# Performance work log

Hardware: AMD Instinct MI355X
Metric: run time of the kernel (lower is better)

Reference implementation:

```python
import jax, jax.numpy as jnp
import numpy as np

B, S, D, E, H, TOPK = 4, 2048, 1024, 32, 128, 4

def setup_inputs() -> dict:
    key = jax.random.key(0)
    k1, k2, k3, k4 = jax.random.split(key, 4)
    x = jax.random.normal(k1, (B, S, D), jnp.float32)
    expert_sel = jax.random.normal(k2, (E, D), jnp.float32) * (D ** -0.5)
    keys = jax.random.normal(k3, (E, D, H), jnp.float32) * (D ** -0.5)
    values = jax.random.normal(k4, (E, H, D), jnp.float32) * (H ** -0.5)
    return {"x": x, "expert_sel": expert_sel, "keys": keys, "values": values, "n_heads": TOPK}

def reference(x, expert_sel, keys, values, n_heads):
    # x: [B,S,D]; expert_sel: [E,D]; keys: [E,D,H]; values: [E,H,D]
    Bv, Sv, Dv = x.shape
    Ev = keys.shape[0]
    xf = x.reshape(-1, Dv)                                  # [N,D]
    N = xf.shape[0]
    gate = jax.nn.sigmoid(xf @ expert_sel.T)                # [N,E] sigmoid gating (sigma-MoE)
    vals, idx = jax.lax.top_k(gate, n_heads)                # [N,k] selected experts + gate weights
    # dense per-token-per-expert gate weights; zero for non-selected experts
    g = jnp.zeros((N, Ev), x.dtype).at[jnp.arange(N)[:, None], idx].set(vals)  # [N,E]
    # grouped expert FFN, expressed densely over the (small) expert axis:
    # out = sum_e g[n,e] * relu(x @ keys[e]) @ values[e]
    h = jax.nn.relu(jnp.einsum('nd,edh->enh', xf, keys))    # [E,N,H]
    out = jnp.einsum('enh,ehd->nd', h * g.T[:, :, None], values)  # [N,D]
    return out.reshape(Bv, Sv, Dv)
```

## Files before the change

kernel.cpp:

```cpp
#include <hip/hip_runtime.h>
#include <hip/hip_bf16.h>

#define NTOK 8192
#define DDIM 1024
#define NEXP 32
#define HDIM 128
#define TOPK 4

typedef __attribute__((ext_vector_type(8))) short bf16x8;
typedef __attribute__((ext_vector_type(4))) float f32x4;

typedef unsigned int uint_g __attribute__((address_space(1)));
typedef unsigned int uint_l __attribute__((address_space(3)));

__device__ __forceinline__ void async_cp16(const void* g, void* l) {
    __builtin_amdgcn_global_load_lds((const uint_g*)g, (uint_l*)l, 16, 0, 0);
}

__device__ inline unsigned short f2bf(float f) {
    unsigned int u = __builtin_bit_cast(unsigned int, f);
    unsigned int r = (u + 0x7fffu + ((u >> 16) & 1u)) >> 16;
    return (unsigned short)r;
}
__device__ inline float bf2f(unsigned short s) {
    unsigned int u = ((unsigned int)s) << 16;
    return __builtin_bit_cast(float, u);
}

__global__ __launch_bounds__(256) void prep_weights(
    const float* __restrict__ x,
    const float* __restrict__ keys, const float* __restrict__ values,
    unsigned short* __restrict__ Kb, unsigned short* __restrict__ Vb,
    unsigned short* __restrict__ Xb)
{
    int idx = blockIdx.x * 256 + threadIdx.x;
    unsigned short o[8];
    if (idx < NEXP * 128 * 128) {
        int n = idx & 127, k0 = (idx >> 7) & 127, e = idx >> 14;
        const float* s = keys + ((size_t)e * DDIM + k0 * 8) * HDIM + n;
        #pragma unroll
        for (int j = 0; j < 8; ++j) o[j] = f2bf(s[(size_t)j * HDIM]);
        *(uint4*)&Kb[(size_t)idx * 8] = *(uint4*)o;
    } else if (idx < 2 * NEXP * 128 * 128) {
        idx -= NEXP * 128 * 128;
        int n = idx & 1023, k0 = (idx >> 10) & 15, e = idx >> 14;
        const float* s = values + ((size_t)e * HDIM + k0 * 8) * DDIM + n;
        #pragma unroll
        for (int j = 0; j < 8; ++j) o[j] = f2bf(s[(size_t)j * DDIM]);
        *(uint4*)&Vb[(size_t)idx * 8] = *(uint4*)o;
    } else {
        idx -= 2 * NEXP * 128 * 128;
        const float* s = x + (size_t)idx * 8;
        #pragma unroll
        for (int j = 0; j < 8; ++j) o[j] = f2bf(s[j]);
        *(uint4*)&Xb[(size_t)idx * 8] = *(uint4*)o;
    }
}

__global__ __launch_bounds__(256) void gate_partial(
    const float* __restrict__ x, const float* __restrict__ es,
    float* __restrict__ gpart)
{
    const int n0    = blockIdx.x * 16;
    const int dbase = blockIdx.y * 256;
    const int tid   = threadIdx.x;

    __shared__ float smem[4608];
    float* Xt  = smem;
    float* Est = smem + 64 * 36;

    const int t4  = (tid & 3) * 4;
    const int e4  = ((tid >> 2) & 7) * 4;
    const int rep = tid >> 5;

    const int xr = tid & 15, xc4 = (tid >> 4) * 4;
    const int er = tid & 31, ec8 = (tid >> 5) * 8;

    float acc[4][4] = {};

    for (int dc = dbase; dc < dbase + 256; dc += 64) {
        __syncthreads();
        {
            float4 v = *(const float4*)&x[(size_t)(n0 + xr) * DDIM + dc + xc4];
            Xt[(xc4 + 0) * 36 + xr] = v.x; Xt[(xc4 + 1) * 36 + xr] = v.y;
            Xt[(xc4 + 2) * 36 + xr] = v.z; Xt[(xc4 + 3) * 36 + xr] = v.w;
        }
        #pragma unroll
        for (int i = 0; i < 2; ++i) {
            float4 v = *(const float4*)&es[(size_t)er * DDIM + dc + ec8 + i * 4];
            Est[(ec8 + i * 4 + 0) * 36 + er] = v.x;
            Est[(ec8 + i * 4 + 1) * 36 + er] = v.y;
            Est[(ec8 + i * 4 + 2) * 36 + er] = v.z;
            Est[(ec8 + i * 4 + 3) * 36 + er] = v.w;
        }
        __syncthreads();

        #pragma unroll
        for (int s = 0; s < 8; ++s) {
            int d = s * 8 + rep;
            float4 xv = *(const float4*)&Xt[d * 36 + t4];
            float4 ev = *(const float4*)&Est[d * 36 + e4];
            const float xa[4] = {xv.x, xv.y, xv.z, xv.w};
            const float ea[4] = {ev.x, ev.y, ev.z, ev.w};
            #pragma unroll
            for (int i = 0; i < 4; ++i)
                #pragma unroll
                for (int j = 0; j < 4; ++j)
                    acc[i][j] = fmaf(xa[i], ea[j], acc[i][j]);
        }
    }

    __syncthreads();
    float* Lp = smem;
    #pragma unroll
    for (int i = 0; i < 4; ++i)
        #pragma unroll
        for (int j = 0; j < 4; ++j)
            Lp[(rep * 16 + t4 + i) * 33 + e4 + j] = acc[i][j];
    __syncthreads();

    for (int p = tid; p < 16 * 32; p += 256) {
        int tok = p >> 5, e = p & 31;
        float s = 0.f;
        #pragma unroll
        for (int r = 0; r < 8; ++r) s += Lp[(r * 16 + tok) * 33 + e];
        gpart[((size_t)blockIdx.y * NTOK + n0 + tok) * NEXP + e] = s;
    }
}

__global__ __launch_bounds__(256) void topk_scatter(
    const float* __restrict__ gpart,
    int* __restrict__ cnt, int* __restrict__ tok_list, float* __restrict__ gates)
{
    const int tid = threadIdx.x;
    const int n   = blockIdx.x * 256 + tid;

    __shared__ int hist[NEXP];
    __shared__ int bbase[NEXP];
    if (tid < NEXP) hist[tid] = 0;

    float lg[NEXP];
    #pragma unroll
    for (int i = 0; i < 8; ++i) {
        float4 v = *(const float4*)&gpart[(size_t)n * NEXP + i * 4];
        lg[i*4+0] = v.x; lg[i*4+1] = v.y; lg[i*4+2] = v.z; lg[i*4+3] = v.w;
    }
    #pragma unroll
    for (int j = 1; j < 4; ++j)
        #pragma unroll
        for (int i = 0; i < 8; ++i) {
            float4 v = *(const float4*)&gpart[((size_t)j * NTOK + n) * NEXP + i * 4];
            lg[i*4+0] += v.x; lg[i*4+1] += v.y; lg[i*4+2] += v.z; lg[i*4+3] += v.w;
        }

    int sel[TOPK]; float sv[TOPK];
    #pragma unroll
    for (int j = 0; j < TOPK; ++j) {
        float bv = -3.0e38f; int bi = 0;
        #pragma unroll
        for (int e = 0; e < NEXP; ++e) {
            bool taken = false;
            #pragma unroll
            for (int q = 0; q < j; ++q) taken = taken || (sel[q] == e);
            float v = taken ? -3.0e38f : lg[e];
            if (v > bv) { bv = v; bi = e; }
        }
        sel[j] = bi; sv[j] = bv;
    }

    __syncthreads();
    int lpos[TOPK];
    #pragma unroll
    for (int j = 0; j < TOPK; ++j) {
        gates[n * TOPK + j] = 1.f / (1.f + expf(-sv[j]));
        lpos[j] = atomicAdd(&hist[sel[j]], 1);
    }
    __syncthreads();
    if (tid < NEXP) bbase[tid] = atomicAdd(&cnt[tid], hist[tid]);
    __syncthreads();
    #pragma unroll
    for (int j = 0; j < TOPK; ++j)
        tok_list[(size_t)sel[j] * NTOK + bbase[sel[j]] + lpos[j]] = n * TOPK + j;
}

__global__ __launch_bounds__(256) void ffn_fused(
    const unsigned short* __restrict__ Xb,
    const unsigned short* __restrict__ Kb,
    const unsigned short* __restrict__ Vb,
    const int* __restrict__ cnt, const int* __restrict__ tok_list,
    const float* __restrict__ gates,
    unsigned short* __restrict__ Ob)
{
    const int bid = blockIdx.x;
    const int e = bid & 31, tile = bid >> 5;
    const int c = cnt[e], base = tile * 64;
    if (base >= c) return;
    const int nt   = min(64, c - base);
    const int tid  = threadIdx.x, wave = tid >> 6, lane = tid & 63;
    const int lm   = lane & 15, quad = lane >> 4;
    const int r2   = (wave >> 1) * 32;
    const int c2   = (wave & 1) * 64;
    const int cw   = (wave & 1) * 32;

    __shared__ __align__(16) unsigned short KV[8192];
    __shared__ __align__(16) unsigned short XO[4608];
    __shared__ __align__(16) unsigned short Hs[64 * 140];
    __shared__ int slot[64]; __shared__ int gtok[64]; __shared__ float gs[64];

    if (tid < 64) {
        if (tid < nt) {
            int v = tok_list[(size_t)e * NTOK + base + tid];
            slot[tid] = v; gtok[tid] = v >> 2; gs[tid] = gates[v];
        } else { slot[tid] = -1; gtok[tid] = 0; gs[tid] = 0.f; }
    }
    __syncthreads();

    const unsigned short* Ke    = Kb + (size_t)e * 131072;
    const unsigned short* Ve    = Vb + (size_t)e * 131072;
    const unsigned short* xrowb = Xb + (size_t)gtok[lane] * DDIM;

    f32x4 acc[2][4];
    #pragma unroll
    for (int i = 0; i < 2; ++i)
        #pragma unroll
        for (int j = 0; j < 4; ++j) acc[i][j] = (f32x4){0.f, 0.f, 0.f, 0.f};

    auto stageA = [&](int t) {
        int dc = t * 64;
        #pragma unroll
        for (int i = 0; i < 4; ++i) {
            int p = wave * 4 + i;
            async_cp16(Ke + ((size_t)(dc / 8 + (p >> 1)) * 128 + (p & 1) * 64 + lane) * 8,
                       &KV[p * 512]);
        }
        #pragma unroll
        for (int i = 0; i < 2; ++i) {
            int k0 = wave * 2 + i;
            async_cp16(xrowb + dc + k0 * 8, &XO[k0 * 512]);
        }
    };

    stageA(0);
    __syncthreads();

    for (int t = 0; t < 16; ++t) {
        #pragma unroll
        for (int ks = 0; ks < 2; ++ks) {
            int k0 = ks * 4 + quad;
            bf16x8 a0 = *(const bf16x8*)&XO[(k0 * 64 + r2 + lm) * 8];
            bf16x8 a1 = *(const bf16x8*)&XO[(k0 * 64 + r2 + 16 + lm) * 8];
            #pragma unroll
            for (int tj = 0; tj < 4; ++tj) {
                bf16x8 bb = *(const bf16x8*)&KV[(k0 * 128 + c2 + tj * 16 + lm) * 8];
                acc[0][tj] = __builtin_amdgcn_mfma_f32_16x16x32_bf16(a0, bb, acc[0][tj], 0, 0, 0);
                acc[1][tj] = __builtin_amdgcn_mfma_f32_16x16x32_bf16(a1, bb, acc[1][tj], 0, 0, 0);
            }
        }
        if (t < 15) {
            __syncthreads();
            stageA(t + 1);
            __syncthreads();
        }
    }

    #pragma unroll
    for (int ti = 0; ti < 2; ++ti)
        #pragma unroll
        for (int reg = 0; reg < 4; ++reg) {
            int m = r2 + ti * 16 + quad * 4 + reg;
            float g = gs[m];
            #pragma unroll
            for (int tj = 0; tj < 4; ++tj)
                Hs[m * 140 + c2 + tj * 16 + lm] = f2bf(fmaxf(acc[ti][tj][reg], 0.f) * g);
        }
    __syncthreads();

    auto stageV = [&](int cc) {
        #pragma unroll
        for (int i = 0; i < 4; ++i) {
            int p = wave * 4 + i;
            async_cp16(Ve + ((size_t)p * 1024 + cc * 64 + lane) * 8, &KV[p * 512]);
        }
    };

    stageV(0);
    __syncthreads();

    const int om = tid >> 2, oq = tid & 3;
    const int os = slot[om];

    for (int cc = 0; cc < 16; ++cc) {
        f32x4 acc2[2][2];
        #pragma unroll
        for (int i = 0; i < 2; ++i) {
            acc2[i][0] = (f32x4){0.f, 0.f, 0.f, 0.f};
            acc2[i][1] = (f32x4){0.f, 0.f, 0.f, 0.f};
        }

        #pragma unroll
        for (int ks = 0; ks < 4; ++ks) {
            int k0 = ks * 4 + quad;
            bf16x8 a0 = *(const bf16x8*)&Hs[(r2 + lm) * 140 + k0 * 8];
            bf16x8 a1 = *(const bf16x8*)&Hs[(r2 + 16 + lm) * 140 + k0 * 8];
            #pragma unroll
            for (int tj = 0; tj < 2; ++tj) {
                bf16x8 bb = *(const bf16x8*)&KV[(k0 * 64 + cw + tj * 16 + lm) * 8];
                acc2[0][tj] = __builtin_amdgcn_mfma_f32_16x16x32_bf16(a0, bb, acc2[0][tj], 0, 0, 0);
                acc2[1][tj] = __builtin_amdgcn_mfma_f32_16x16x32_bf16(a1, bb, acc2[1][tj], 0, 0, 0);
            }
        }

        #pragma unroll
        for (int ti = 0; ti < 2; ++ti)
            #pragma unroll
            for (int reg = 0; reg < 4; ++reg) {
                int m = r2 + ti * 16 + quad * 4 + reg;
                XO[m * 72 + cw + lm]      = f2bf(acc2[ti][0][reg]);
                XO[m * 72 + cw + 16 + lm] = f2bf(acc2[ti][1][reg]);
            }
        __syncthreads();

        if (os >= 0) {
            uint4 v0 = *(const uint4*)&XO[om * 72 + oq * 16];
            uint4 v1 = *(const uint4*)&XO[om * 72 + oq * 16 + 8];
            unsigned short* op = Ob + (size_t)os * DDIM + cc * 64 + oq * 16;
            *(uint4*)op       = v0;
            *(uint4*)(op + 8) = v1;
        }
        if (cc < 15) stageV(cc + 1);
        __syncthreads();
    }
}

__global__ __launch_bounds__(256) void reduce_out(
    const unsigned short* __restrict__ Ob, float* __restrict__ out)
{
    const int tid = threadIdx.x;
    const int n   = blockIdx.x * 2 + (tid >> 7);
    const int cc  = (tid & 127) * 8;

    float s[8] = {};
    #pragma unroll
    for (int j = 0; j < 4; ++j) {
        uint4 v = *(const uint4*)&Ob[((size_t)n * 4 + j) * DDIM + cc];
        const unsigned int w[4] = {v.x, v.y, v.z, v.w};
        #pragma unroll
        for (int q = 0; q < 4; ++q) {
            s[q * 2 + 0] += bf2f((unsigned short)(w[q] & 0xffff));
            s[q * 2 + 1] += bf2f((unsigned short)(w[q] >> 16));
        }
    }
    float4 o0 = {s[0], s[1], s[2], s[3]};
    float4 o1 = {s[4], s[5], s[6], s[7]};
    *(float4*)&out[(size_t)n * DDIM + cc]     = o0;
    *(float4*)&out[(size_t)n * DDIM + cc + 4] = o1;
}

extern "C" void kernel_launch(void* const* d_in, const int* in_sizes, int n_in,
                              void* d_out, int out_size, void* d_ws, size_t ws_size,
                              hipStream_t stream) {
    const float* x      = (const float*)d_in[0];
    const float* es     = (const float*)d_in[1];
    const float* keys   = (const float*)d_in[2];
    const float* values = (const float*)d_in[3];
    float* out          = (float*)d_out;

    char* w = (char*)d_ws;
    int*   cnt      = (int*)w;               w += 256;
    int*   tok_list = (int*)w;               w += (size_t)NEXP * NTOK * sizeof(int);
    float* gates    = (float*)w;             w += (size_t)NTOK * TOPK * sizeof(float);
    float* gpart    = (float*)w;             w += (size_t)4 * NTOK * NEXP * sizeof(float);
    unsigned short* Kb = (unsigned short*)w; w += (size_t)NEXP * 128 * 128 * 8 * 2;
    unsigned short* Vb = (unsigned short*)w; w += (size_t)NEXP * 16 * 1024 * 8 * 2;
    unsigned short* Xb = (unsigned short*)w; w += (size_t)NTOK * DDIM * 2;
    unsigned short* Ob = (unsigned short*)w;

    hipMemsetAsync(cnt, 0, NEXP * sizeof(int), stream);

    prep_weights<<<8192, 256, 0, stream>>>(x, keys, values, Kb, Vb, Xb);
    gate_partial<<<dim3(NTOK / 16, 4), 256, 0, stream>>>(x, es, gpart);
    topk_scatter<<<NTOK / 256, 256, 0, stream>>>(gpart, cnt, tok_list, gates);

    ffn_fused<<<128 * NEXP, 256, 0, stream>>>(Xb, Kb, Vb, cnt, tok_list, gates, Ob);
    reduce_out<<<NTOK / 2, 256, 0, stream>>>(Ob, out);
}
```

Baseline: 205.9 us.

## Double-buffer FFN stages, persistent expert tiles, fuse x bf16 cast into gating

The x-to-bf16 conversion moves out of prep_weights and into gate_partial, which already stages x in shared memory, so x is read from global memory once instead of twice. ffn_fused becomes persistent: 512 blocks each loop over tiles of one expert with a stride of 16, replacing the 4096-block grid where most blocks exited early. The K/X, V and output staging buffers are double-buffered in one shared arena, so async loads of the next chunk overlap the MFMA work and one barrier per step is removed. The larger shared footprint (about 76 KB) may lower occupancy, and the new buffer aliasing needs careful barrier placement.

```diff
diff --git a/kernel.cpp b/kernel.cpp
--- a/kernel.cpp
+++ b/kernel.cpp
@@ -28,10 +28,8 @@
 }
 
 __global__ __launch_bounds__(256) void prep_weights(
-    const float* __restrict__ x,
     const float* __restrict__ keys, const float* __restrict__ values,
-    unsigned short* __restrict__ Kb, unsigned short* __restrict__ Vb,
-    unsigned short* __restrict__ Xb)
+    unsigned short* __restrict__ Kb, unsigned short* __restrict__ Vb)
 {
     int idx = blockIdx.x * 256 + threadIdx.x;
     unsigned short o[8];
@@ -41,25 +39,20 @@
         #pragma unroll
         for (int j = 0; j < 8; ++j) o[j] = f2bf(s[(size_t)j * HDIM]);
         *(uint4*)&Kb[(size_t)idx * 8] = *(uint4*)o;
-    } else if (idx < 2 * NEXP * 128 * 128) {
+    } else {
         idx -= NEXP * 128 * 128;
         int n = idx & 1023, k0 = (idx >> 10) & 15, e = idx >> 14;
         const float* s = values + ((size_t)e * HDIM + k0 * 8) * DDIM + n;
         #pragma unroll
         for (int j = 0; j < 8; ++j) o[j] = f2bf(s[(size_t)j * DDIM]);
         *(uint4*)&Vb[(size_t)idx * 8] = *(uint4*)o;
-    } else {
-        idx -= 2 * NEXP * 128 * 128;
-        const float* s = x + (size_t)idx * 8;
-        #pragma unroll
-        for (int j = 0; j < 8; ++j) o[j] = f2bf(s[j]);
-        *(uint4*)&Xb[(size_t)idx * 8] = *(uint4*)o;
     }
 }
 
 __global__ __launch_bounds__(256) void gate_partial(
     const float* __restrict__ x, const float* __restrict__ es,
-    float* __restrict__ gpart)
+    float* __restrict__ gpart,
+    unsigned short* __restrict__ Xb)
 {
     const int n0    = blockIdx.x * 16;
     const int dbase = blockIdx.y * 256;
@@ -75,6 +68,8 @@
 
     const int xr = tid & 15, xc4 = (tid >> 4) * 4;
     const int er = tid & 31, ec8 = (tid >> 5) * 8;
+
+    const int ctok = tid >> 4, cd4 = (tid & 15) * 4;
 
     float acc[4][4] = {};
 
@@ -94,6 +89,13 @@
             Est[(ec8 + i * 4 + 3) * 36 + er] = v.w;
         }
         __syncthreads();
+
+        {
+            unsigned short o[4];
+            #pragma unroll
+            for (int j = 0; j < 4; ++j) o[j] = f2bf(Xt[(cd4 + j) * 36 + ctok]);
+            *(uint2*)&Xb[(size_t)(n0 + ctok) * DDIM + dc + cd4] = *(uint2*)o;
+        }
 
         #pragma unroll
         for (int s = 0; s < 8; ++s) {
@@ -192,122 +194,76 @@
     unsigned short* __restrict__ Ob)
 {
     const int bid = blockIdx.x;
-    const int e = bid & 31, tile = bid >> 5;
-    const int c = cnt[e], base = tile * 64;
-    if (base >= c) return;
-    const int nt   = min(64, c - base);
+    const int e = bid & 31, t0 = bid >> 5;
+    const int c = cnt[e];
     const int tid  = threadIdx.x, wave = tid >> 6, lane = tid & 63;
     const int lm   = lane & 15, quad = lane >> 4;
     const int r2   = (wave >> 1) * 32;
     const int c2   = (wave & 1) * 64;
     const int cw   = (wave & 1) * 32;
 
-    __shared__ __align__(16) unsigned short KV[8192];
-    __shared__ __align__(16) unsigned short XO[4608];
-    __shared__ __align__(16) unsigned short Hs[64 * 140];
+    __shared__ __align__(16) unsigned short P[37888];
     __shared__ int slot[64]; __shared__ int gtok[64]; __shared__ float gs[64];
 
-    if (tid < 64) {
-        if (tid < nt) {
-            int v = tok_list[(size_t)e * NTOK + base + tid];
-            slot[tid] = v; gtok[tid] = v >> 2; gs[tid] = gates[v];
-        } else { slot[tid] = -1; gtok[tid] = 0; gs[tid] = 0.f; }
-    }
-    __syncthreads();
-
-    const unsigned short* Ke    = Kb + (size_t)e * 131072;
-    const unsigned short* Ve    = Vb + (size_t)e * 131072;
-    const unsigned short* xrowb = Xb + (size_t)gtok[lane] * DDIM;
-
-    f32x4 acc[2][4];
-    #pragma unroll
-    for (int i = 0; i < 2; ++i)
-        #pragma unroll
-        for (int j = 0; j < 4; ++j) acc[i][j] = (f32x4){0.f, 0.f, 0.f, 0.f};
-
-    auto stageA = [&](int t) {
-        int dc = t * 64;
-        #pragma unroll
-        for (int i = 0; i < 4; ++i) {
-            int p = wave * 4 + i;
-            async_cp16(Ke + ((size_t)(dc / 8 + (p >> 1)) * 128 + (p & 1) * 64 + lane) * 8,
-                       &KV[p * 512]);
-        }
-        #pragma unroll
-        for (int i = 0; i < 2; ++i) {
-            int k0 = wave * 2 + i;
-            async_cp16(xrowb + dc + k0 * 8, &XO[k0 * 512]);
-        }
-    };
-
-    stageA(0);
-    __syncthreads();
-
-    for (int t = 0; t < 16; ++t) {
-        #pragma unroll
-        for (int ks = 0; ks < 2; ++ks) {
-            int k0 = ks * 4 + quad;
-            bf16x8 a0 = *(const bf16x8*)&XO[(k0 * 64 + r2 + lm) * 8];
-            bf16x8 a1 = *(const bf16x8*)&XO[(k0 * 64 + r2 + 16 + lm) * 8];
-            #pragma unroll
-            for (int tj = 0; tj < 4; ++tj) {
-                bf16x8 bb = *(const bf16x8*)&KV[(k0 * 128 + c2 + tj * 16 + lm) * 8];
-                acc[0][tj] = __builtin_amdgcn_mfma_f32_16x16x32_bf16(a0, bb, acc[0][tj], 0, 0, 0);
-                acc[1][tj] = __builtin_amdgcn_mfma_f32_16x16x32_bf16(a1, bb, acc[1][tj], 0, 0, 0);
-            }
-        }
-        if (t < 15) {
+    const unsigned short* Ke = Kb + (size_t)e * 131072;
+    const unsigned short* Ve = Vb + (size_t)e * 131072;
+
+    for (int tile = t0; tile * 64 < c; tile += 16) {
+        const int base = tile * 64;
+        const int nt   = min(64, c - base);
+
+        __syncthreads();
+        if (tid < 64) {
+            if (tid < nt) {
+                int v = tok_list[(size_t)e * NTOK + base + tid];
+                slot[tid] = v; gtok[tid] = v >> 2; gs[tid] = gates[v];
+            } else { slot[tid] = -1; gtok[tid] = 0; gs[tid] = 0.f; }
+        }
+        __syncthreads();
+
+        const unsigned short* xrowb = Xb + (size_t)gtok[lane] * DDIM;
+
+        f32x4 acc[2][4];
+        #pragma unroll
+        for (int i = 0; i < 2; ++i)
+            #pragma unroll
+            for (int j = 0; j < 4; ++j) acc[i][j] = (f32x4){0.f, 0.f, 0.f, 0.f};
+
+        auto stageA = [&](int t, int cb) {
+            unsigned short* B = &P[cb * 12288];
+            #pragma unroll
+            for (int i = 0; i < 4; ++i) {
+                int p = wave * 4 + i;
+                async_cp16(Ke + ((size_t)(t * 8 + (p >> 1)) * 128 + (p & 1) * 64 + lane) * 8,
+                           B + p * 512);
+            }
+            #pragma unroll
+            for (int i = 0; i < 2; ++i) {
+                int k0 = wave * 2 + i;
+                async_cp16(xrowb + t * 64 + k0 * 8, B + 8192 + k0 * 512);
+            }
+        };
+
+        stageA(0, 0);
+        __syncthreads();
+
+        for (int t = 0; t < 16; ++t) {
+            const int cb = t & 1;
+            if (t < 15) stageA(t + 1, cb ^ 1);
+            const unsigned short* B = &P[cb * 12288];
+            #pragma unroll
+            for (int ks = 0; ks < 2; ++ks) {
+                int k0 = ks * 4 + quad;
+                bf16x8 a0 = *(const bf16x8*)&B[8192 + (k0 * 64 + r2 + lm) * 8];
+                bf16x8 a1 = *(const bf16x8*)&B[8192 + (k0 * 64 + r2 + 16 + lm) * 8];
+                #pragma unroll
+                for (int tj = 0; tj < 4; ++tj) {
+                    bf16x8 bb = *(const bf16x8*)&B[(k0 * 128 + c2 + tj * 16 + lm) * 8];
+                    acc[0][tj] = __builtin_amdgcn_mfma_f32_16x16x32_bf16(a0, bb, acc[0][tj], 0, 0, 0);
+                    acc[1][tj] = __builtin_amdgcn_mfma_f32_16x16x32_bf16(a1, bb, acc[1][tj], 0, 0, 0);
+                }
+            }
             __syncthreads();
-            stageA(t + 1);
-            __syncthreads();
-        }
-    }
-
-    #pragma unroll
-    for (int ti = 0; ti < 2; ++ti)
-        #pragma unroll
-        for (int reg = 0; reg < 4; ++reg) {
-            int m = r2 + ti * 16 + quad * 4 + reg;
-            float g = gs[m];
-            #pragma unroll
-            for (int tj = 0; tj < 4; ++tj)
-                Hs[m * 140 + c2 + tj * 16 + lm] = f2bf(fmaxf(acc[ti][tj][reg], 0.f) * g);
-        }
-    __syncthreads();
-
-    auto stageV = [&](int cc) {
-        #pragma unroll
-        for (int i = 0; i < 4; ++i) {
-            int p = wave * 4 + i;
-            async_cp16(Ve + ((size_t)p * 1024 + cc * 64 + lane) * 8, &KV[p * 512]);
-        }
-    };
-
-    stageV(0);
-    __syncthreads();
-
-    const int om = tid >> 2, oq = tid & 3;
-    const int os = slot[om];
-
-    for (int cc = 0; cc < 16; ++cc) {
-        f32x4 acc2[2][2];
-        #pragma unroll
-        for (int i = 0; i < 2; ++i) {
-            acc2[i][0] = (f32x4){0.f, 0.f, 0.f, 0.f};
-            acc2[i][1] = (f32x4){0.f, 0.f, 0.f, 0.f};
-        }
-
-        #pragma unroll
-        for (int ks = 0; ks < 4; ++ks) {
-            int k0 = ks * 4 + quad;
-            bf16x8 a0 = *(const bf16x8*)&Hs[(r2 + lm) * 140 + k0 * 8];
-            bf16x8 a1 = *(const bf16x8*)&Hs[(r2 + 16 + lm) * 140 + k0 * 8];
-            #pragma unroll
-            for (int tj = 0; tj < 2; ++tj) {
-                bf16x8 bb = *(const bf16x8*)&KV[(k0 * 64 + cw + tj * 16 + lm) * 8];
-                acc2[0][tj] = __builtin_amdgcn_mfma_f32_16x16x32_bf16(a0, bb, acc2[0][tj], 0, 0, 0);
-                acc2[1][tj] = __builtin_amdgcn_mfma_f32_16x16x32_bf16(a1, bb, acc2[1][tj], 0, 0, 0);
-            }
         }
 
         #pragma unroll
@@ -315,20 +271,71 @@
             #pragma unroll
             for (int reg = 0; reg < 4; ++reg) {
                 int m = r2 + ti * 16 + quad * 4 + reg;
-                XO[m * 72 + cw + lm]      = f2bf(acc2[ti][0][reg]);
-                XO[m * 72 + cw + 16 + lm] = f2bf(acc2[ti][1][reg]);
-            }
-        __syncthreads();
-
-        if (os >= 0) {
-            uint4 v0 = *(const uint4*)&XO[om * 72 + oq * 16];
-            uint4 v1 = *(const uint4*)&XO[om * 72 + oq * 16 + 8];
-            unsigned short* op = Ob + (size_t)os * DDIM + cc * 64 + oq * 16;
-            *(uint4*)op       = v0;
-            *(uint4*)(op + 8) = v1;
-        }
-        if (cc < 15) stageV(cc + 1);
-        __syncthreads();
+                float g = gs[m];
+                #pragma unroll
+                for (int tj = 0; tj < 4; ++tj)
+                    P[m * 140 + c2 + tj * 16 + lm] = f2bf(fmaxf(acc[ti][tj][reg], 0.f) * g);
+            }
+
+        auto stageV = [&](int cc, int vb) {
+            unsigned short* B = &P[12288 + vb * 8192];
+            #pragma unroll
+            for (int i = 0; i < 4; ++i) {
+                int p = wave * 4 + i;
+                async_cp16(Ve + ((size_t)p * 1024 + cc * 64 + lane) * 8, B + p * 512);
+            }
+        };
+
+        stageV(0, 0);
+        __syncthreads();
+
+        const int om = tid >> 2, oq = tid & 3;
+        const int os = slot[om];
+
+        for (int cc = 0; cc < 16; ++cc) {
+            const int vb = cc & 1;
+            if (cc < 15) stageV(cc + 1, vb ^ 1);
+
+            f32x4 acc2[2][2];
+            #pragma unroll
+            for (int i = 0; i < 2; ++i) {
+                acc2[i][0] = (f32x4){0.f, 0.f, 0.f, 0.f};
+                acc2[i][1] = (f32x4){0.f, 0.f, 0.f, 0.f};
+            }
+
+            const unsigned short* B = &P[12288 + vb * 8192];
+            #pragma unroll
+            for (int ks = 0; ks < 4; ++ks) {
+                int k0 = ks * 4 + quad;
+                bf16x8 a0 = *(const bf16x8*)&P[(r2 + lm) * 140 + k0 * 8];
+                bf16x8 a1 = *(const bf16x8*)&P[(r2 + 16 + lm) * 140 + k0 * 8];
+                #pragma unroll
+                for (int tj = 0; tj < 2; ++tj) {
+                    bf16x8 bb = *(const bf16x8*)&B[(k0 * 64 + cw + tj * 16 + lm) * 8];
+                    acc2[0][tj] = __builtin_amdgcn_mfma_f32_16x16x32_bf16(a0, bb, acc2[0][tj], 0, 0, 0);
+                    acc2[1][tj] = __builtin_amdgcn_mfma_f32_16x16x32_bf16(a1, bb, acc2[1][tj], 0, 0, 0);
+                }
+            }
+
+            unsigned short* OSB = &P[28672 + vb * 4608];
+            #pragma unroll
+            for (int ti = 0; ti < 2; ++ti)
+                #pragma unroll
+                for (int reg = 0; reg < 4; ++reg) {
+                    int m = r2 + ti * 16 + quad * 4 + reg;
+                    OSB[m * 72 + cw + lm]      = f2bf(acc2[ti][0][reg]);
+                    OSB[m * 72 + cw + 16 + lm] = f2bf(acc2[ti][1][reg]);
+                }
+            __syncthreads();
+
+            if (os >= 0) {
+                uint4 v0 = *(const uint4*)&OSB[om * 72 + oq * 16];
+                uint4 v1 = *(const uint4*)&OSB[om * 72 + oq * 16 + 8];
+                unsigned short* op = Ob + (size_t)os * DDIM + cc * 64 + oq * 16;
+                *(uint4*)op       = v0;
+                *(uint4*)(op + 8) = v1;
+            }
+        }
     }
 }
 
@@ -377,10 +384,10 @@
 
     hipMemsetAsync(cnt, 0, NEXP * sizeof(int), stream);
 
-    prep_weights<<<8192, 256, 0, stream>>>(x, keys, values, Kb, Vb, Xb);
-    gate_partial<<<dim3(NTOK / 16, 4), 256, 0, stream>>>(x, es, gpart);
+    prep_weights<<<4096, 256, 0, stream>>>(keys, values, Kb, Vb);
+    gate_partial<<<dim3(NTOK / 16, 4), 256, 0, stream>>>(x, es, gpart, Xb);
     topk_scatter<<<NTOK / 256, 256, 0, stream>>>(gpart, cnt, tok_list, gates);
 
-    ffn_fused<<<128 * NEXP, 256, 0, stream>>>(Xb, Kb, Vb, cnt, tok_list, gates, Ob);
+    ffn_fused<<<512, 256, 0, stream>>>(Xb, Kb, Vb, cnt, tok_list, gates, Ob);
     reduce_out<<<NTOK / 2, 256, 0, stream>>>(Ob, out);
 }
```

After: 248.8 us. +20.8%, slower.

## Fuse weight prep, gate logits, top-k and scatter into one kernel

Applied to the files above, without the earlier changes.

Merges the weight conversion, gating GEMM and top-k/scatter kernels into a single launch. Weight-conversion blocks run alongside gate blocks, and each gate block now covers the full D dimension for 16 tokens. Each gate block also writes the bf16 copy of x while x is in shared memory. This removes the gpart partial-logit buffer round trip, two kernel launches and a separate pass over x. In exchange there are fewer gate blocks doing 4x more serial work each, and only 16 threads per block do the top-k, so the global atomics on cnt go from one batch per 256 tokens to one per 16 tokens.

```diff
diff --git a/kernel.cpp b/kernel.cpp
--- a/kernel.cpp
+++ b/kernel.cpp
@@ -27,47 +27,44 @@
     return __builtin_bit_cast(float, u);
 }
 
-__global__ __launch_bounds__(256) void prep_weights(
-    const float* __restrict__ x,
+__global__ __launch_bounds__(256) void prep_gate(
+    const float* __restrict__ x, const float* __restrict__ es,
     const float* __restrict__ keys, const float* __restrict__ values,
     unsigned short* __restrict__ Kb, unsigned short* __restrict__ Vb,
-    unsigned short* __restrict__ Xb)
+    unsigned short* __restrict__ Xb,
+    int* __restrict__ cnt, int* __restrict__ tok_list, float* __restrict__ gates)
 {
-    int idx = blockIdx.x * 256 + threadIdx.x;
-    unsigned short o[8];
-    if (idx < NEXP * 128 * 128) {
-        int n = idx & 127, k0 = (idx >> 7) & 127, e = idx >> 14;
-        const float* s = keys + ((size_t)e * DDIM + k0 * 8) * HDIM + n;
-        #pragma unroll
-        for (int j = 0; j < 8; ++j) o[j] = f2bf(s[(size_t)j * HDIM]);
-        *(uint4*)&Kb[(size_t)idx * 8] = *(uint4*)o;
-    } else if (idx < 2 * NEXP * 128 * 128) {
-        idx -= NEXP * 128 * 128;
-        int n = idx & 1023, k0 = (idx >> 10) & 15, e = idx >> 14;
-        const float* s = values + ((size_t)e * HDIM + k0 * 8) * DDIM + n;
-        #pragma unroll
-        for (int j = 0; j < 8; ++j) o[j] = f2bf(s[(size_t)j * DDIM]);
-        *(uint4*)&Vb[(size_t)idx * 8] = *(uint4*)o;
-    } else {
-        idx -= 2 * NEXP * 128 * 128;
-        const float* s = x + (size_t)idx * 8;
-        #pragma unroll
-        for (int j = 0; j < 8; ++j) o[j] = f2bf(s[j]);
-        *(uint4*)&Xb[(size_t)idx * 8] = *(uint4*)o;
-    }
-}
-
-__global__ __launch_bounds__(256) void gate_partial(
-    const float* __restrict__ x, const float* __restrict__ es,
-    float* __restrict__ gpart)
-{
-    const int n0    = blockIdx.x * 16;
-    const int dbase = blockIdx.y * 256;
-    const int tid   = threadIdx.x;
+    const int tid = threadIdx.x;
+
+    if (blockIdx.x < 4096) {
+        int idx = blockIdx.x * 256 + tid;
+        unsigned short o[8];
+        if (idx < NEXP * 128 * 128) {
+            int n = idx & 127, k0 = (idx >> 7) & 127, e = idx >> 14;
+            const float* s = keys + ((size_t)e * DDIM + k0 * 8) * HDIM + n;
+            #pragma unroll
+            for (int j = 0; j < 8; ++j) o[j] = f2bf(s[(size_t)j * HDIM]);
+            *(uint4*)&Kb[(size_t)idx * 8] = *(uint4*)o;
+        } else {
+            idx -= NEXP * 128 * 128;
+            int n = idx & 1023, k0 = (idx >> 10) & 15, e = idx >> 14;
+            const float* s = values + ((size_t)e * HDIM + k0 * 8) * DDIM + n;
+            #pragma unroll
+            for (int j = 0; j < 8; ++j) o[j] = f2bf(s[(size_t)j * DDIM]);
+            *(uint4*)&Vb[(size_t)idx * 8] = *(uint4*)o;
+        }
+        return;
+    }
+
+    const int n0 = (int)(blockIdx.x - 4096) * 16;
 
     __shared__ float smem[4608];
+    __shared__ float Ls[16 * 33];
+    __shared__ int hist[NEXP];
+    __shared__ int bbase[NEXP];
     float* Xt  = smem;
     float* Est = smem + 64 * 36;
+    float* Lp  = smem;
 
     const int t4  = (tid & 3) * 4;
     const int e4  = ((tid >> 2) & 7) * 4;
@@ -76,111 +73,111 @@
     const int xr = tid & 15, xc4 = (tid >> 4) * 4;
     const int er = tid & 31, ec8 = (tid >> 5) * 8;
 
-    float acc[4][4] = {};
-
-    for (int dc = dbase; dc < dbase + 256; dc += 64) {
+    const int ctok = tid >> 4, cd4 = (tid & 15) * 4;
+
+    const int rtok = tid >> 5, re = tid & 31;
+
+    float lsum[2] = {0.f, 0.f};
+
+    if (tid < NEXP) hist[tid] = 0;
+
+    for (int q = 0; q < 4; ++q) {
+        float acc[4][4] = {};
+
+        for (int dc = q * 256; dc < q * 256 + 256; dc += 64) {
+            __syncthreads();
+            {
+                float4 v = *(const float4*)&x[(size_t)(n0 + xr) * DDIM + dc + xc4];
+                Xt[(xc4 + 0) * 36 + xr] = v.x; Xt[(xc4 + 1) * 36 + xr] = v.y;
+                Xt[(xc4 + 2) * 36 + xr] = v.z; Xt[(xc4 + 3) * 36 + xr] = v.w;
+            }
+            #pragma unroll
+            for (int i = 0; i < 2; ++i) {
+                float4 v = *(const float4*)&es[(size_t)er * DDIM + dc + ec8 + i * 4];
+                Est[(ec8 + i * 4 + 0) * 36 + er] = v.x;
+                Est[(ec8 + i * 4 + 1) * 36 + er] = v.y;
+                Est[(ec8 + i * 4 + 2) * 36 + er] = v.z;
+                Est[(ec8 + i * 4 + 3) * 36 + er] = v.w;
+            }
+            __syncthreads();
+
+            {
+                unsigned short o[4];
+                #pragma unroll
+                for (int j = 0; j < 4; ++j) o[j] = f2bf(Xt[(cd4 + j) * 36 + ctok]);
+                *(uint2*)&Xb[(size_t)(n0 + ctok) * DDIM + dc + cd4] = *(uint2*)o;
+            }
+
+            #pragma unroll
+            for (int s = 0; s < 8; ++s) {
+                int d = s * 8 + rep;
+                float4 xv = *(const float4*)&Xt[d * 36 + t4];
+                float4 ev = *(const float4*)&Est[d * 36 + e4];
+                const float xa[4] = {xv.x, xv.y, xv.z, xv.w};
+                const float ea[4] = {ev.x, ev.y, ev.z, ev.w};
+                #pragma unroll
+                for (int i = 0; i < 4; ++i)
+                    #pragma unroll
+                    for (int j = 0; j < 4; ++j)
+                        acc[i][j] = fmaf(xa[i], ea[j], acc[i][j]);
+            }
+        }
+
         __syncthreads();
-        {
-            float4 v = *(const float4*)&x[(size_t)(n0 + xr) * DDIM + dc + xc4];
-            Xt[(xc4 + 0) * 36 + xr] = v.x; Xt[(xc4 + 1) * 36 + xr] = v.y;
-            Xt[(xc4 + 2) * 36 + xr] = v.z; Xt[(xc4 + 3) * 36 + xr] = v.w;
-        }
-        #pragma unroll
-        for (int i = 0; i < 2; ++i) {
-            float4 v = *(const float4*)&es[(size_t)er * DDIM + dc + ec8 + i * 4];
-            Est[(ec8 + i * 4 + 0) * 36 + er] = v.x;
-            Est[(ec8 + i * 4 + 1) * 36 + er] = v.y;
-            Est[(ec8 + i * 4 + 2) * 36 + er] = v.z;
-            Est[(ec8 + i * 4 + 3) * 36 + er] = v.w;
-        }
+        #pragma unroll
+        for (int i = 0; i < 4; ++i)
+            #pragma unroll
+            for (int j = 0; j < 4; ++j)
+                Lp[(rep * 16 + t4 + i) * 33 + e4 + j] = acc[i][j];
         __syncthreads();
 
         #pragma unroll
-        for (int s = 0; s < 8; ++s) {
-            int d = s * 8 + rep;
-            float4 xv = *(const float4*)&Xt[d * 36 + t4];
-            float4 ev = *(const float4*)&Est[d * 36 + e4];
-            const float xa[4] = {xv.x, xv.y, xv.z, xv.w};
-            const float ea[4] = {ev.x, ev.y, ev.z, ev.w};
-            #pragma unroll
-            for (int i = 0; i < 4; ++i)
+        for (int h = 0; h < 2; ++h) {
+            int tok = rtok + h * 8;
+            float s = 0.f;
+            #pragma unroll
+            for (int r = 0; r < 8; ++r) s += Lp[(r * 16 + tok) * 33 + re];
+            lsum[h] += s;
+        }
+    }
+
+    #pragma unroll
+    for (int h = 0; h < 2; ++h) Ls[(rtok + h * 8) * 33 + re] = lsum[h];
+    __syncthreads();
+
+    int sel[TOPK]; int lpos[TOPK];
+    if (tid < 16) {
+        float lg[NEXP];
+        #pragma unroll
+        for (int e2 = 0; e2 < NEXP; ++e2) lg[e2] = Ls[tid * 33 + e2];
+        float sv[TOPK];
+        #pragma unroll
+        for (int j = 0; j < TOPK; ++j) {
+            float bv = -3.0e38f; int bi = 0;
+            #pragma unroll
+            for (int e2 = 0; e2 < NEXP; ++e2) {
+                bool taken = false;
                 #pragma unroll
-                for (int j = 0; j < 4; ++j)
-                    acc[i][j] = fmaf(xa[i], ea[j], acc[i][j]);
-        }
-    }
-
-    __syncthreads();
-    float* Lp = smem;
-    #pragma unroll
-    for (int i = 0; i < 4; ++i)
-        #pragma unroll
-        for (int j = 0; j < 4; ++j)
-            Lp[(rep * 16 + t4 + i) * 33 + e4 + j] = acc[i][j];
-    __syncthreads();
-
-    for (int p = tid; p < 16 * 32; p += 256) {
-        int tok = p >> 5, e = p & 31;
-        float s = 0.f;
-        #pragma unroll
-        for (int r = 0; r < 8; ++r) s += Lp[(r * 16 + tok) * 33 + e];
-        gpart[((size_t)blockIdx.y * NTOK + n0 + tok) * NEXP + e] = s;
-    }
-}
-
-__global__ __launch_bounds__(256) void topk_scatter(
-    const float* __restrict__ gpart,
-    int* __restrict__ cnt, int* __restrict__ tok_list, float* __restrict__ gates)
-{
-    const int tid = threadIdx.x;
-    const int n   = blockIdx.x * 256 + tid;
-
-    __shared__ int hist[NEXP];
-    __shared__ int bbase[NEXP];
-    if (tid < NEXP) hist[tid] = 0;
-
-    float lg[NEXP];
-    #pragma unroll
-    for (int i = 0; i < 8; ++i) {
-        float4 v = *(const float4*)&gpart[(size_t)n * NEXP + i * 4];
-        lg[i*4+0] = v.x; lg[i*4+1] = v.y; lg[i*4+2] = v.z; lg[i*4+3] = v.w;
-    }
-    #pragma unroll
-    for (int j = 1; j < 4; ++j)
-        #pragma unroll
-        for (int i = 0; i < 8; ++i) {
-            float4 v = *(const float4*)&gpart[((size_t)j * NTOK + n) * NEXP + i * 4];
-            lg[i*4+0] += v.x; lg[i*4+1] += v.y; lg[i*4+2] += v.z; lg[i*4+3] += v.w;
-        }
-
-    int sel[TOPK]; float sv[TOPK];
-    #pragma unroll
-    for (int j = 0; j < TOPK; ++j) {
-        float bv = -3.0e38f; int bi = 0;
-        #pragma unroll
-        for (int e = 0; e < NEXP; ++e) {
-            bool taken = false;
-            #pragma unroll
-            for (int q = 0; q < j; ++q) taken = taken || (sel[q] == e);
-            float v = taken ? -3.0e38f : lg[e];
-            if (v > bv) { bv = v; bi = e; }
-        }
-        sel[j] = bi; sv[j] = bv;
-    }
-
-    __syncthreads();
-    int lpos[TOPK];
-    #pragma unroll
-    for (int j = 0; j < TOPK; ++j) {
-        gates[n * TOPK + j] = 1.f / (1.f + expf(-sv[j]));
-        lpos[j] = atomicAdd(&hist[sel[j]], 1);
+                for (int q = 0; q < j; ++q) taken = taken || (sel[q] == e2);
+                float v = taken ? -3.0e38f : lg[e2];
+                if (v > bv) { bv = v; bi = e2; }
+            }
+            sel[j] = bi; sv[j] = bv;
+        }
+        #pragma unroll
+        for (int j = 0; j < TOPK; ++j) {
+            gates[(size_t)(n0 + tid) * TOPK + j] = 1.f / (1.f + expf(-sv[j]));
+            lpos[j] = atomicAdd(&hist[sel[j]], 1);
+        }
     }
     __syncthreads();
     if (tid < NEXP) bbase[tid] = atomicAdd(&cnt[tid], hist[tid]);
     __syncthreads();
-    #pragma unroll
-    for (int j = 0; j < TOPK; ++j)
-        tok_list[(size_t)sel[j] * NTOK + bbase[sel[j]] + lpos[j]] = n * TOPK + j;
+    if (tid < 16) {
+        #pragma unroll
+        for (int j = 0; j < TOPK; ++j)
+            tok_list[(size_t)sel[j] * NTOK + bbase[sel[j]] + lpos[j]] = (n0 + tid) * TOPK + j;
+    }
 }
 
 __global__ __launch_bounds__(256) void ffn_fused(
@@ -369,7 +366,6 @@
     int*   cnt      = (int*)w;               w += 256;
     int*   tok_list = (int*)w;               w += (size_t)NEXP * NTOK * sizeof(int);
     float* gates    = (float*)w;             w += (size_t)NTOK * TOPK * sizeof(float);
-    float* gpart    = (float*)w;             w += (size_t)4 * NTOK * NEXP * sizeof(float);
     unsigned short* Kb = (unsigned short*)w; w += (size_t)NEXP * 128 * 128 * 8 * 2;
     unsigned short* Vb = (unsigned short*)w; w += (size_t)NEXP * 16 * 1024 * 8 * 2;
     unsigned short* Xb = (unsigned short*)w; w += (size_t)NTOK * DDIM * 2;
@@ -377,10 +373,8 @@
 
     hipMemsetAsync(cnt, 0, NEXP * sizeof(int), stream);
 
-    prep_weights<<<8192, 256, 0, stream>>>(x, keys, values, Kb, Vb, Xb);
-    gate_partial<<<dim3(NTOK / 16, 4), 256, 0, stream>>>(x, es, gpart);
-    topk_scatter<<<NTOK / 256, 256, 0, stream>>>(gpart, cnt, tok_list, gates);
-
+    prep_gate<<<4096 + NTOK / 16, 256, 0, stream>>>(x, es, keys, values, Kb, Vb, Xb,
+                                                    cnt, tok_list, gates);
     ffn_fused<<<128 * NEXP, 256, 0, stream>>>(Xb, Kb, Vb, cnt, tok_list, gates, Ob);
     reduce_out<<<NTOK / 2, 256, 0, stream>>>(Ob, out);
 }
```

After: 213.3 us. +3.6%, slower.
